# Kernel tuning notes

Measured on AMD Instinct MI355X. Metric: run time of the kernel, lower is better.

The kernel has to match this reference:

```python
import jax, jax.numpy as jnp
import numpy as np

N_NODES = 100000
N_EDGES = 3200000
D_IN = 256
D_OUT = 256


def setup_inputs() -> dict:
    key = jax.random.key(0)
    k1, k2, k3, k4, k5, k6 = jax.random.split(key, 6)
    x = jax.random.normal(k1, (N_NODES, D_IN), dtype=jnp.float32)
    edge_row = jax.random.randint(k2, (N_EDGES,), 0, N_NODES, dtype=jnp.int32)
    edge_col = jax.random.randint(k3, (N_EDGES,), 0, N_NODES, dtype=jnp.int32)
    edge_val = jax.random.uniform(k4, (N_EDGES,), dtype=jnp.float32)
    # nn.Linear params (PyTorch stores weight as [out, in]; we apply x @ W.T + b)
    bound = 1.0 / np.sqrt(D_IN)
    W = jax.random.uniform(k5, (D_OUT, D_IN), minval=-bound, maxval=bound, dtype=jnp.float32)
    b = jax.random.uniform(k6, (D_OUT,), minval=-bound, maxval=bound, dtype=jnp.float32)
    return {"x": x, "edge_row": edge_row, "edge_col": edge_col,
            "edge_val": edge_val, "W": W, "b": b}


def reference(x, edge_row, edge_col, edge_val, W, b):
    # SpMM: agg[i] = sum over edges e with row[e]==i of val[e] * x[col[e]]
    messages = edge_val[:, None] * x[edge_col]          # [E, D_in]
    agg = jax.ops.segment_sum(messages, edge_row, num_segments=N_NODES)  # [N, D_in]
    # Dense linear: agg @ W.T + b
    return jnp.einsum('nd,od->no', agg, W) + b
```

## Files before the change

kernel.cpp:

```cpp
#include <hip/hip_runtime.h>

#define THREADS 256
#define P2T 512
#define P1B 1024
#define MAXEPB 3200
#define CVTXB 1536

typedef __attribute__((ext_vector_type(8))) short short8;
typedef __attribute__((ext_vector_type(4))) float f32x4;

__device__ __forceinline__ unsigned short f2bf(float f) {
    unsigned u = __builtin_bit_cast(unsigned, f);
    return (unsigned short)((u + 0x7FFFu + ((u >> 16) & 1u)) >> 16);
}
__device__ __forceinline__ float bf2f_lo(unsigned u) { return __builtin_bit_cast(float, u << 16); }
__device__ __forceinline__ float bf2f_hi(unsigned u) { return __builtin_bit_cast(float, u & 0xFFFF0000u); }

__global__ __launch_bounds__(THREADS)
void p1_presort_kernel(const int* __restrict__ row, const int* __restrict__ col,
                       const float* __restrict__ val, int* __restrict__ gcur,
                       uint2* __restrict__ estage, int n_edges, int nbkt, int capS) {
    __shared__ int h[512];
    __shared__ int base[512];
    __shared__ int gchunk[512];
    __shared__ int curl[512];
    __shared__ int wsum[4];
    __shared__ uint2 rec[MAXEPB];
    __shared__ unsigned short rbkt[MAXEPB];

    int b = blockIdx.x, tid = threadIdx.x;
    int g = b & 7;
    int E0 = (int)((long long)b * n_edges / P1B);
    int E1 = (int)((long long)(b + 1) * n_edges / P1B);
    int cnt = E1 - E0;

    h[2 * tid] = 0; h[2 * tid + 1] = 0;
    __syncthreads();
    for (int e = E0 + tid; e < E1; e += THREADS)
        atomicAdd(&h[row[e] >> 8], 1);
    __syncthreads();
    int v0 = h[2 * tid], v1 = h[2 * tid + 1];
    int ts = v0 + v1;
    int lane = tid & 63, w = tid >> 6;
    int incl = ts;
    #pragma unroll
    for (int off = 1; off < 64; off <<= 1) {
        int t = __shfl_up(incl, off, 64);
        if (lane >= off) incl += t;
    }
    if (lane == 63) wsum[w] = incl;
    __syncthreads();
    int wo = 0;
    for (int i = 0; i < w; ++i) wo += wsum[i];
    int excl = wo + incl - ts;
    base[2 * tid] = excl;
    base[2 * tid + 1] = excl + v0;
    curl[2 * tid] = excl;
    curl[2 * tid + 1] = excl + v0;
    #pragma unroll
    for (int q = 0; q < 2; ++q) {
        int bk = 2 * tid + q;
        if (bk < nbkt) {
            int c = h[bk];
            int ro = c ? atomicAdd(&gcur[bk * 8 + g], c) : 0;
            gchunk[bk] = (bk * 8 + g) * capS + ro;
        }
    }
    __syncthreads();
    for (int e = E0 + tid; e < E1; e += THREADS) {
        int r = row[e];
        int bk = r >> 8;
        int pos = atomicAdd(&curl[bk], 1);
        rec[pos] = make_uint2(((unsigned)(r & 255) << 24) | (unsigned)col[e],
                              (unsigned)__float_as_int(val[e]));
        rbkt[pos] = (unsigned short)bk;
    }
    __syncthreads();
    for (int i = tid; i < cnt; i += THREADS) {
        int bk = rbkt[i];
        int dst = gchunk[bk] + (i - base[bk]);
        if (dst < (bk * 8 + g + 1) * capS)
            estage[dst] = rec[i];
    }
}

__global__ void cvtWX_kernel(const float* __restrict__ W, unsigned short* __restrict__ WbP,
                             const float4* __restrict__ x, uint4* __restrict__ xb, int n8) {
    int b = blockIdx.x, tid = threadIdx.x;
    if (b < 32) {
        int f = b * THREADS + tid;
        int l = f & 63, nt = (f >> 6) & 15, k0i = f >> 10;
        int r = nt * 16 + (l & 15);
        int koff = k0i * 32 + 8 * (l >> 4);
        const float4* s = reinterpret_cast<const float4*>(W + r * 256 + koff);
        float4 a = s[0], bb = s[1];
        uint4 o;
        o.x = (unsigned)f2bf(a.x) | ((unsigned)f2bf(a.y) << 16);
        o.y = (unsigned)f2bf(a.z) | ((unsigned)f2bf(a.w) << 16);
        o.z = (unsigned)f2bf(bb.x) | ((unsigned)f2bf(bb.y) << 16);
        o.w = (unsigned)f2bf(bb.z) | ((unsigned)f2bf(bb.w) << 16);
        reinterpret_cast<uint4*>(WbP)[f] = o;
    } else {
        int stride = CVTXB * THREADS;
        for (int i = (b - 32) * THREADS + tid; i < n8; i += stride) {
            float4 a = x[2 * i], bb = x[2 * i + 1];
            uint4 o;
            o.x = (unsigned)f2bf(a.x) | ((unsigned)f2bf(a.y) << 16);
            o.y = (unsigned)f2bf(a.z) | ((unsigned)f2bf(a.w) << 16);
            o.z = (unsigned)f2bf(bb.x) | ((unsigned)f2bf(bb.y) << 16);
            o.w = (unsigned)f2bf(bb.z) | ((unsigned)f2bf(bb.w) << 16);
            reinterpret_cast<uint4*>(xb)[i] = o;
        }
    }
}

__global__ void p2_sort(const uint2* __restrict__ estage, const int* __restrict__ gcur,
                        int2* __restrict__ pr, int* __restrict__ offs,
                        int capS, int n_nodes, int nbkt) {
    __shared__ int red[P2T];
    __shared__ int h[256];
    __shared__ int curh[256];
    __shared__ int wsum[4];
    __shared__ int scnt[8];
    int b = blockIdx.x, tid = threadIdx.x;

    int lim = b * 8;
    int partial = 0;
    for (int j = tid; j < lim; j += P2T) {
        int c = gcur[j];
        partial += c > capS ? capS : c;
    }
    red[tid] = partial;
    __syncthreads();
    #pragma unroll
    for (int s = P2T / 2; s > 0; s >>= 1) {
        if (tid < s) red[tid] += red[tid + s];
        __syncthreads();
    }
    int gb = red[0];
    if (tid < 8) {
        int c = gcur[b * 8 + tid];
        scnt[tid] = c > capS ? capS : c;
    }
    if (tid < 256) h[tid] = 0;
    __syncthreads();

    #pragma unroll
    for (int g = 0; g < 8; ++g) {
        int cnt = scnt[g];
        int base = (b * 8 + g) * capS;
        for (int i = tid; i < cnt; i += P2T)
            atomicAdd(&h[estage[base + i].x >> 24], 1);
    }
    __syncthreads();
    if (tid < 256) {
        int v = h[tid];
        int lane = tid & 63, w = tid >> 6;
        int incl = v;
        #pragma unroll
        for (int off = 1; off < 64; off <<= 1) {
            int t = __shfl_up(incl, off, 64);
            if (lane >= off) incl += t;
        }
        if (lane == 63) wsum[w] = incl;
        __syncthreads();
        int wo = 0;
        for (int i = 0; i < w; ++i) wo += wsum[i];
        int excl = wo + incl - v;
        int node = b * 256 + tid;
        if (node < n_nodes) offs[node] = gb + excl;
        curh[tid] = gb + excl;
    } else {
        __syncthreads();
    }
    if (b == nbkt - 1 && tid == 0) {
        int t = 0;
        #pragma unroll
        for (int g = 0; g < 8; ++g) t += scnt[g];
        offs[n_nodes] = gb + t;
    }
    __syncthreads();
    #pragma unroll
    for (int g = 0; g < 8; ++g) {
        int cnt = scnt[g];
        int base = (b * 8 + g) * capS;
        for (int i = tid; i < cnt; i += P2T) {
            uint2 p = estage[base + i];
            int q = atomicAdd(&curh[(int)(p.x >> 24)], 1);
            pr[q] = make_int2((int)(p.x & 0x00FFFFFFu), (int)p.y);
        }
    }
}

template<int OUT_BF16>
__global__ void spmm_bf16_kernel(const uint2* __restrict__ xb, const int* __restrict__ offs,
                                 const int2* __restrict__ pr, void* __restrict__ outp,
                                 int b0, int b1, int nnodes) {
    int g = blockIdx.x & 7;
    int inst = blockIdx.x >> 3;
    int bkt = b0 + g + 8 * (inst >> 6);
    if (bkt >= b1) return;
    int wid = bkt * 256 + (inst & 63) * 4 + (threadIdx.x >> 6);
    int lane = threadIdx.x & 63;
    if (wid >= nnodes) return;
    int s = offs[wid], e = offs[wid + 1];
    float a0 = 0.f, a1 = 0.f, a2 = 0.f, a3 = 0.f;
    int i = s;
    if (i < e && (i & 1)) {
        int2 p = pr[i];
        uint2 xv = xb[(size_t)p.x * 64 + lane];
        float v = __int_as_float(p.y);
        a0 = fmaf(v, bf2f_lo(xv.x), a0); a1 = fmaf(v, bf2f_hi(xv.x), a1);
        a2 = fmaf(v, bf2f_lo(xv.y), a2); a3 = fmaf(v, bf2f_hi(xv.y), a3);
        ++i;
    }
    for (; i + 8 <= e; i += 8) {
        int4 pa = *reinterpret_cast<const int4*>(pr + i);
        int4 pb = *reinterpret_cast<const int4*>(pr + i + 2);
        int4 pc = *reinterpret_cast<const int4*>(pr + i + 4);
        int4 pd = *reinterpret_cast<const int4*>(pr + i + 6);
        uint2 x0 = xb[(size_t)pa.x * 64 + lane];
        uint2 x1 = xb[(size_t)pa.z * 64 + lane];
        uint2 x2 = xb[(size_t)pb.x * 64 + lane];
        uint2 x3 = xb[(size_t)pb.z * 64 + lane];
        uint2 x4_ = xb[(size_t)pc.x * 64 + lane];
        uint2 x5 = xb[(size_t)pc.z * 64 + lane];
        uint2 x6 = xb[(size_t)pd.x * 64 + lane];
        uint2 x7 = xb[(size_t)pd.z * 64 + lane];
        float v0 = __int_as_float(pa.y), v1 = __int_as_float(pa.w);
        float v2 = __int_as_float(pb.y), v3 = __int_as_float(pb.w);
        float v4 = __int_as_float(pc.y), v5 = __int_as_float(pc.w);
        float v6 = __int_as_float(pd.y), v7 = __int_as_float(pd.w);
        a0 = fmaf(v0, bf2f_lo(x0.x), a0); a1 = fmaf(v0, bf2f_hi(x0.x), a1);
        a2 = fmaf(v0, bf2f_lo(x0.y), a2); a3 = fmaf(v0, bf2f_hi(x0.y), a3);
        a0 = fmaf(v1, bf2f_lo(x1.x), a0); a1 = fmaf(v1, bf2f_hi(x1.x), a1);
        a2 = fmaf(v1, bf2f_lo(x1.y), a2); a3 = fmaf(v1, bf2f_hi(x1.y), a3);
        a0 = fmaf(v2, bf2f_lo(x2.x), a0); a1 = fmaf(v2, bf2f_hi(x2.x), a1);
        a2 = fmaf(v2, bf2f_lo(x2.y), a2); a3 = fmaf(v2, bf2f_hi(x2.y), a3);
        a0 = fmaf(v3, bf2f_lo(x3.x), a0); a1 = fmaf(v3, bf2f_hi(x3.x), a1);
        a2 = fmaf(v3, bf2f_lo(x3.y), a2); a3 = fmaf(v3, bf2f_hi(x3.y), a3);
        a0 = fmaf(v4, bf2f_lo(x4_.x), a0); a1 = fmaf(v4, bf2f_hi(x4_.x), a1);
        a2 = fmaf(v4, bf2f_lo(x4_.y), a2); a3 = fmaf(v4, bf2f_hi(x4_.y), a3);
        a0 = fmaf(v5, bf2f_lo(x5.x), a0); a1 = fmaf(v5, bf2f_hi(x5.x), a1);
        a2 = fmaf(v5, bf2f_lo(x5.y), a2); a3 = fmaf(v5, bf2f_hi(x5.y), a3);
        a0 = fmaf(v6, bf2f_lo(x6.x), a0); a1 = fmaf(v6, bf2f_hi(x6.x), a1);
        a2 = fmaf(v6, bf2f_lo(x6.y), a2); a3 = fmaf(v6, bf2f_hi(x6.y), a3);
        a0 = fmaf(v7, bf2f_lo(x7.x), a0); a1 = fmaf(v7, bf2f_hi(x7.x), a1);
        a2 = fmaf(v7, bf2f_lo(x7.y), a2); a3 = fmaf(v7, bf2f_hi(x7.y), a3);
    }
    for (; i + 2 <= e; i += 2) {
        int4 pa = *reinterpret_cast<const int4*>(pr + i);
        uint2 x0 = xb[(size_t)pa.x * 64 + lane];
        uint2 x1 = xb[(size_t)pa.z * 64 + lane];
        float v0 = __int_as_float(pa.y), v1 = __int_as_float(pa.w);
        a0 = fmaf(v0, bf2f_lo(x0.x), a0); a1 = fmaf(v0, bf2f_hi(x0.x), a1);
        a2 = fmaf(v0, bf2f_lo(x0.y), a2); a3 = fmaf(v0, bf2f_hi(x0.y), a3);
        a0 = fmaf(v1, bf2f_lo(x1.x), a0); a1 = fmaf(v1, bf2f_hi(x1.x), a1);
        a2 = fmaf(v1, bf2f_lo(x1.y), a2); a3 = fmaf(v1, bf2f_hi(x1.y), a3);
    }
    for (; i < e; ++i) {
        int2 p = pr[i];
        uint2 xv = xb[(size_t)p.x * 64 + lane];
        float v = __int_as_float(p.y);
        a0 = fmaf(v, bf2f_lo(xv.x), a0); a1 = fmaf(v, bf2f_hi(xv.x), a1);
        a2 = fmaf(v, bf2f_lo(xv.y), a2); a3 = fmaf(v, bf2f_hi(xv.y), a3);
    }
    if (OUT_BF16) {
        ushort4 o;
        o.x = f2bf(a0); o.y = f2bf(a1); o.z = f2bf(a2); o.w = f2bf(a3);
        *reinterpret_cast<ushort4*>((unsigned short*)outp + (size_t)wid * 256 + 4 * lane) = o;
    } else {
        ((float4*)outp)[(size_t)wid * 64 + lane] = make_float4(a0, a1, a2, a3);
    }
}

__global__ void spmm_f32_kernel(const float4* __restrict__ x4, const int* __restrict__ offs,
                                const int2* __restrict__ pr, float4* __restrict__ out4,
                                int nnodes) {
    int wid = (blockIdx.x * blockDim.x + threadIdx.x) >> 6;
    int lane = threadIdx.x & 63;
    if (wid >= nnodes) return;
    int s = offs[wid], e = offs[wid + 1];
    float4 acc = make_float4(0.f, 0.f, 0.f, 0.f);
    for (int i = s; i < e; ++i) {
        int2 p = pr[i];
        float4 xv = x4[(size_t)p.x * 64 + lane];
        float v = __int_as_float(p.y);
        acc.x = fmaf(v, xv.x, acc.x); acc.y = fmaf(v, xv.y, acc.y);
        acc.z = fmaf(v, xv.z, acc.z); acc.w = fmaf(v, xv.w, acc.w);
    }
    out4[(size_t)wid * 64 + lane] = acc;
}

__launch_bounds__(256)
__global__ void gemm_direct3_kernel(const unsigned short* __restrict__ aggb,
                                    const unsigned short* __restrict__ WbP,
                                    const float* __restrict__ bias,
                                    float* __restrict__ out, int n) {
    int tid = threadIdx.x, lane = tid & 63, w = tid >> 6;
    int row0 = blockIdx.x * 128 + w * 32;
    int lr = lane & 15, lg = lane >> 4;
    const unsigned short* arow0 = aggb + (size_t)(row0 + lr) * 256 + lg * 8;
    const unsigned short* arow1 = arow0 + 16 * 256;
    short8 af0[8], af1[8];
    #pragma unroll
    for (int k = 0; k < 8; ++k) {
        af0[k] = *reinterpret_cast<const short8*>(arow0 + k * 32);
        af1[k] = *reinterpret_cast<const short8*>(arow1 + k * 32);
    }
    #pragma unroll
    for (int half = 0; half < 2; ++half) {
        f32x4 acc0[8], acc1[8];
        #pragma unroll
        for (int nt = 0; nt < 8; ++nt) {
            acc0[nt] = (f32x4){0.f, 0.f, 0.f, 0.f};
            acc1[nt] = (f32x4){0.f, 0.f, 0.f, 0.f};
        }
        #pragma unroll
        for (int k = 0; k < 8; ++k) {
            #pragma unroll
            for (int nt = 0; nt < 8; ++nt) {
                short8 bf_ = *reinterpret_cast<const short8*>(
                    &WbP[(size_t)((k * 16 + half * 8 + nt) * 64 + lane) * 8]);
                acc0[nt] = __builtin_amdgcn_mfma_f32_16x16x32_bf16(af0[k], bf_, acc0[nt], 0, 0, 0);
                acc1[nt] = __builtin_amdgcn_mfma_f32_16x16x32_bf16(af1[k], bf_, acc1[nt], 0, 0, 0);
            }
        }
        #pragma unroll
        for (int nt = 0; nt < 8; ++nt) {
            int gc = half * 128 + nt * 16 + lr;
            float bv = bias[gc];
            #pragma unroll
            for (int q = 0; q < 4; ++q) {
                int gr0 = row0 + lg * 4 + q;
                int gr1 = gr0 + 16;
                if (gr0 < n) out[(size_t)gr0 * 256 + gc] = acc0[nt][q] + bv;
                if (gr1 < n) out[(size_t)gr1 * 256 + gc] = acc1[nt][q] + bv;
            }
        }
    }
}


__global__ void zero_kernel(int* __restrict__ p, int n) {
    int i = blockIdx.x * blockDim.x + threadIdx.x;
    if (i < n) p[i] = 0;
}

__global__ void hist_part_kernel(const int* __restrict__ row, int* __restrict__ cnt,
                                 int n_edges, int n_nodes) {
    int g = blockIdx.x & 7;
    int inst = blockIdx.x >> 3;
    int ninst = gridDim.x >> 3;
    int lo = (int)(((long long)g * n_nodes) >> 3);
    int hi = (int)(((long long)(g + 1) * n_nodes) >> 3);
    int e0 = (int)(((long long)inst * n_edges) / ninst);
    int e1 = (int)(((long long)(inst + 1) * n_edges) / ninst);
    for (int e = e0 + threadIdx.x; e < e1; e += THREADS) {
        int r = row[e];
        if (r >= lo && r < hi) atomicAdd(&cnt[r], 1);
    }
}

__global__ void place_part_kernel(const int* __restrict__ row, const int* __restrict__ col,
                                  const float* __restrict__ val, int* __restrict__ cur,
                                  int2* __restrict__ pr, int n_edges, int n_nodes) {
    int g = blockIdx.x & 7;
    int inst = blockIdx.x >> 3;
    int ninst = gridDim.x >> 3;
    int lo = (int)(((long long)g * n_nodes) >> 3);
    int hi = (int)(((long long)(g + 1) * n_nodes) >> 3);
    int e0 = (int)(((long long)inst * n_edges) / ninst);
    int e1 = (int)(((long long)(inst + 1) * n_edges) / ninst);
    for (int e = e0 + threadIdx.x; e < e1; e += THREADS) {
        int r = row[e];
        if (r >= lo && r < hi) {
            int p = atomicAdd(&cur[r], 1);
            pr[p] = make_int2(col[e], __float_as_int(val[e]));
        }
    }
}

__global__ void scan1_kernel(const int* __restrict__ cnt, int* __restrict__ offs,
                             int* __restrict__ bsum, int n) {
    int tid = threadIdx.x;
    int base = blockIdx.x * 1024 + tid * 4;
    int v0 = 0, v1 = 0, v2 = 0, v3 = 0;
    if (base + 3 < n) {
        int4 v = *reinterpret_cast<const int4*>(cnt + base);
        v0 = v.x; v1 = v.y; v2 = v.z; v3 = v.w;
    } else {
        if (base + 0 < n) v0 = cnt[base + 0];
        if (base + 1 < n) v1 = cnt[base + 1];
        if (base + 2 < n) v2 = cnt[base + 2];
    }
    int ts = v0 + v1 + v2 + v3;
    int lane = tid & 63;
    int incl = ts;
    #pragma unroll
    for (int off = 1; off < 64; off <<= 1) {
        int t = __shfl_up(incl, off, 64);
        if (lane >= off) incl += t;
    }
    __shared__ int wsum[4];
    int w = tid >> 6;
    if (lane == 63) wsum[w] = incl;
    __syncthreads();
    int wo = 0;
    for (int i = 0; i < w; ++i) wo += wsum[i];
    int excl = wo + incl - ts;
    if (base + 0 < n) offs[base + 0] = excl;
    if (base + 1 < n) offs[base + 1] = excl + v0;
    if (base + 2 < n) offs[base + 2] = excl + v0 + v1;
    if (base + 3 < n) offs[base + 3] = excl + v0 + v1 + v2;
    if (tid == THREADS - 1) bsum[blockIdx.x] = wo + incl;
}

__global__ void scan2_kernel(int* __restrict__ bsum, int nb) {
    int tid = threadIdx.x;
    int base = tid * 4;
    int v0 = 0, v1 = 0, v2 = 0, v3 = 0;
    if (base + 0 < nb) v0 = bsum[base + 0];
    if (base + 1 < nb) v1 = bsum[base + 1];
    if (base + 2 < nb) v2 = bsum[base + 2];
    if (base + 3 < nb) v3 = bsum[base + 3];
    int ts = v0 + v1 + v2 + v3;
    int lane = tid & 63;
    int incl = ts;
    #pragma unroll
    for (int off = 1; off < 64; off <<= 1) {
        int t = __shfl_up(incl, off, 64);
        if (lane >= off) incl += t;
    }
    __shared__ int wsum[4];
    int w = tid >> 6;
    if (lane == 63) wsum[w] = incl;
    __syncthreads();
    int wo = 0;
    for (int i = 0; i < w; ++i) wo += wsum[i];
    int excl = wo + incl - ts;
    if (base + 0 < nb) bsum[base + 0] = excl;
    if (base + 1 < nb) bsum[base + 1] = excl + v0;
    if (base + 2 < nb) bsum[base + 2] = excl + v0 + v1;
    if (base + 3 < nb) bsum[base + 3] = excl + v0 + v1 + v2;
    if (tid == THREADS - 1) bsum[nb] = wo + incl;
}

__global__ void scan3_kernel(int* __restrict__ offs, const int* __restrict__ bsum,
                             int* __restrict__ cur, int n) {
    int i = blockIdx.x * blockDim.x + threadIdx.x;
    if (i < n) {
        int v = offs[i] + bsum[i >> 10];
        offs[i] = v;
        cur[i] = v;
    }
    if (i == 0) offs[n] = bsum[(n + 1023) >> 10];
}

__global__ void cvt_bf16_kernel(const float4* __restrict__ in, uint4* __restrict__ out, int n8) {
    int i = blockIdx.x * blockDim.x + threadIdx.x;
    if (i >= n8) return;
    float4 a = in[2 * i], b = in[2 * i + 1];
    uint4 o;
    o.x = (unsigned)f2bf(a.x) | ((unsigned)f2bf(a.y) << 16);
    o.y = (unsigned)f2bf(a.z) | ((unsigned)f2bf(a.w) << 16);
    o.z = (unsigned)f2bf(b.x) | ((unsigned)f2bf(b.y) << 16);
    o.w = (unsigned)f2bf(b.z) | ((unsigned)f2bf(b.w) << 16);
    out[i] = o;
}

__launch_bounds__(256, 2)
__global__ void gemm_mfma_kernel(float* __restrict__ out, const unsigned short* __restrict__ Wb,
                                 const float* __restrict__ bias, int nrows) {
    __shared__ unsigned short As[64][264];
    __shared__ unsigned short Ws[256][40];
    int tid = threadIdx.x;
    int rowBase = blockIdx.x * 64;

    const float4* o4 = reinterpret_cast<const float4*>(out);
    for (int it = tid; it < 64 * 64; it += 256) {
        int r = it >> 6, c = it & 63;
        float4 v = make_float4(0.f, 0.f, 0.f, 0.f);
        int gr = rowBase + r;
        if (gr < nrows) v = o4[(size_t)gr * 64 + c];
        ushort4 w;
        w.x = f2bf(v.x); w.y = f2bf(v.y); w.z = f2bf(v.z); w.w = f2bf(v.w);
        *reinterpret_cast<ushort4*>(&As[r][c * 4]) = w;
    }

    int w = tid >> 6, lane = tid & 63;
    int lr = lane & 15, lg = lane >> 4;
    f32x4 acc[16];
    #pragma unroll
    for (int nt = 0; nt < 16; ++nt) acc[nt] = (f32x4){0.f, 0.f, 0.f, 0.f};

    for (int k0 = 0; k0 < 256; k0 += 32) {
        __syncthreads();
        for (int it = tid; it < 1024; it += 256) {
            int r = it >> 2, c = it & 3;
            uint4 v = *reinterpret_cast<const uint4*>(Wb + (size_t)r * 256 + k0 + c * 8);
            *reinterpret_cast<uint4*>(&Ws[r][c * 8]) = v;
        }
        __syncthreads();
        short8 af = *reinterpret_cast<const short8*>(&As[w * 16 + lr][k0 + 8 * lg]);
        #pragma unroll
        for (int nt = 0; nt < 16; ++nt) {
            short8 bf_ = *reinterpret_cast<const short8*>(&Ws[nt * 16 + lr][8 * lg]);
            acc[nt] = __builtin_amdgcn_mfma_f32_16x16x32_bf16(af, bf_, acc[nt], 0, 0, 0);
        }
    }

    #pragma unroll
    for (int nt = 0; nt < 16; ++nt) {
        int gc = nt * 16 + lr;
        float bv = bias[gc];
        #pragma unroll
        for (int q = 0; q < 4; ++q) {
            int gr = rowBase + w * 16 + lg * 4 + q;
            if (gr < nrows) out[(size_t)gr * 256 + gc] = acc[nt][q] + bv;
        }
    }
}


extern "C" void kernel_launch(void* const* d_in, const int* in_sizes, int n_in,
                              void* d_out, int out_size, void* d_ws, size_t ws_size,
                              hipStream_t stream) {
    const float* x     = (const float*)d_in[0];
    const int*   erow  = (const int*)d_in[1];
    const int*   ecol  = (const int*)d_in[2];
    const float* evalv = (const float*)d_in[3];
    const float* W     = (const float*)d_in[4];
    const float* bias  = (const float*)d_in[5];
    float* out = (float*)d_out;

    int n_nodes = in_sizes[0] / 256;
    int n_edges = in_sizes[1];

    int nbkt = (n_nodes + 255) >> 8;
    int avg8 = n_edges / (8 * (nbkt > 0 ? nbkt : 1)) + 1;
    int capS = avg8 + avg8 / 8 + 512;

    size_t A = (size_t)((n_nodes + 63) & ~63) + 64;
    int* offs  = (int*)d_ws;
    int* gcur  = offs + A;
    unsigned short* WbP = (unsigned short*)(gcur + 4096);
    int2* pr = (int2*)(WbP + 65536);
    int* after_pr = (int*)(pr + n_edges);

    size_t est_ints  = (size_t)nbkt * 8 * capS * 2;
    size_t aggb_ints = (size_t)n_nodes * 128 + 32768;
    size_t xb_ints   = (size_t)n_nodes * 128;
    size_t alias_ints = est_ints > aggb_ints ? est_ints : aggb_ints;
    size_t head_ints = (size_t)(after_pr - (int*)d_ws);
    size_t need_new = (head_ints + alias_ints + xb_ints) * 4;
    bool new_ok = (nbkt <= 512) && (nbkt >= 1) && (n_nodes <= (1 << 24)) &&
                  (n_edges <= P1B * (MAXEPB - 64)) && ws_size >= need_new;

    if (new_ok) {
        uint2* estage = (uint2*)after_pr;
        unsigned short* aggb = (unsigned short*)after_pr;
        unsigned short* xb = (unsigned short*)(after_pr + alias_ints);

        hipMemsetAsync(gcur, 0, 4096 * sizeof(int), stream);
        int n8 = n_nodes * 32;
        cvtWX_kernel<<<32 + CVTXB, THREADS, 0, stream>>>(
            W, WbP, (const float4*)x, (uint4*)xb, n8);
        p1_presort_kernel<<<P1B, THREADS, 0, stream>>>(
            erow, ecol, evalv, gcur, estage, n_edges, nbkt, capS);
        p2_sort<<<nbkt, P2T, 0, stream>>>(estage, gcur, pr, offs, capS, n_nodes, nbkt);

        int grid = 8 * ((nbkt + 7) / 8) * 64;
        spmm_bf16_kernel<1><<<grid, THREADS, 0, stream>>>(
            (const uint2*)xb, offs, pr, aggb, 0, nbkt, n_nodes);
        int gb = (n_nodes + 127) / 128;
        gemm_direct3_kernel<<<gb, THREADS, 0, stream>>>(aggb, WbP, bias, out, n_nodes);
    } else {
        int nb = (n_nodes + 1023) >> 10;
        size_t Af = (size_t)((n_nodes + 63) & ~63);
        int* cnt   = (int*)d_ws;
        int* offsf = cnt + Af;
        int* cur   = offsf + Af;
        int* bsum  = cur + Af;
        int* wbase = bsum + (((size_t)nb + 64) & ~63ull);
        unsigned short* Wbf = (unsigned short*)wbase;
        int2* prf  = (int2*)(Wbf + 65536);
        int* aft   = (int*)(prf + n_edges);
        unsigned short* xbf = (unsigned short*)aft;
        size_t need_old = (size_t)((char*)(xbf + (size_t)n_nodes * 256) - (char*)d_ws);
        bool told = ws_size >= need_old;

        zero_kernel<<<(n_nodes + THREADS - 1) / THREADS, THREADS, 0, stream>>>(cnt, n_nodes);
        hist_part_kernel<<<2048, THREADS, 0, stream>>>(erow, cnt, n_edges, n_nodes);
        scan1_kernel<<<nb, THREADS, 0, stream>>>(cnt, offsf, bsum, n_nodes);
        scan2_kernel<<<1, THREADS, 0, stream>>>(bsum, nb);
        scan3_kernel<<<(n_nodes + THREADS - 1) / THREADS, THREADS, 0, stream>>>(offsf, bsum, cur, n_nodes);
        place_part_kernel<<<2048, THREADS, 0, stream>>>(erow, ecol, evalv, cur, prf, n_edges, n_nodes);
        cvt_bf16_kernel<<<32, THREADS, 0, stream>>>((const float4*)W, (uint4*)Wbf, 65536 / 8);

        int gb = (n_nodes + 63) / 64;
        if (told) {
            int n8 = n_nodes * 32;
            cvt_bf16_kernel<<<(n8 + THREADS - 1) / THREADS, THREADS, 0, stream>>>(
                (const float4*)x, (uint4*)xbf, n8);
            int nbf = (n_nodes + 255) / 256;
            int gridf = 8 * ((nbf + 7) / 8) * 64;
            spmm_bf16_kernel<0><<<gridf, THREADS, 0, stream>>>(
                (const uint2*)xbf, offsf, prf, out, 0, nbf, n_nodes);
        } else {
            int spmm_blocks_f = (n_nodes + 3) / 4;
            spmm_f32_kernel<<<spmm_blocks_f, THREADS, 0, stream>>>(
                (const float4*)x, offsf, prf, (float4*)out, n_nodes);
        }
        gemm_mfma_kernel<<<gb, THREADS, 0, stream>>>(out, Wbf, bias, n_nodes);
    }
}
```

Baseline: 422.9 us.

## Slice bf16 features into 16 column slabs for cache-resident sliced SpMM

Converts x to bf16 in a feature-sliced layout of 16 slabs, each holding 16 columns (32 bytes per node), so every slab is about 3.2 MB and can stay in L2/LLC. The SpMM runs per slice, with 8 edges handled in parallel per wave and a shuffle reduction at the end. Its output uses the same sliced layout, and the GEMM's A-fragment loads are changed to read it. The aim is to turn random 512-byte row gathers from a 51 MB table into cache-friendly 32-byte gathers. In exchange, the edge list is re-read 16 times and the reduction adds shuffle overhead.

```diff
diff --git a/kernel.cpp b/kernel.cpp
--- a/kernel.cpp
+++ b/kernel.cpp
@@ -85,7 +85,8 @@
 }
 
 __global__ void cvtWX_kernel(const float* __restrict__ W, unsigned short* __restrict__ WbP,
-                             const float4* __restrict__ x, uint4* __restrict__ xb, int n8) {
+                             const float* __restrict__ x, unsigned short* __restrict__ xs,
+                             int n_nodes) {
     int b = blockIdx.x, tid = threadIdx.x;
     if (b < 32) {
         int f = b * THREADS + tid;
@@ -102,14 +103,23 @@
         reinterpret_cast<uint4*>(WbP)[f] = o;
     } else {
         int stride = CVTXB * THREADS;
-        for (int i = (b - 32) * THREADS + tid; i < n8; i += stride) {
-            float4 a = x[2 * i], bb = x[2 * i + 1];
-            uint4 o;
-            o.x = (unsigned)f2bf(a.x) | ((unsigned)f2bf(a.y) << 16);
-            o.y = (unsigned)f2bf(a.z) | ((unsigned)f2bf(a.w) << 16);
-            o.z = (unsigned)f2bf(bb.x) | ((unsigned)f2bf(bb.y) << 16);
-            o.w = (unsigned)f2bf(bb.z) | ((unsigned)f2bf(bb.w) << 16);
-            reinterpret_cast<uint4*>(xb)[i] = o;
+        int total = n_nodes * 16;
+        for (int idx = (b - 32) * THREADS + tid; idx < total; idx += stride) {
+            int s = idx / n_nodes;
+            int n = idx - s * n_nodes;
+            const float4* xr = reinterpret_cast<const float4*>(x) + (size_t)n * 64 + s * 4;
+            float4 a = xr[0], bb = xr[1], c = xr[2], d = xr[3];
+            uint4 o0, o1;
+            o0.x = (unsigned)f2bf(a.x) | ((unsigned)f2bf(a.y) << 16);
+            o0.y = (unsigned)f2bf(a.z) | ((unsigned)f2bf(a.w) << 16);
+            o0.z = (unsigned)f2bf(bb.x) | ((unsigned)f2bf(bb.y) << 16);
+            o0.w = (unsigned)f2bf(bb.z) | ((unsigned)f2bf(bb.w) << 16);
+            o1.x = (unsigned)f2bf(c.x) | ((unsigned)f2bf(c.y) << 16);
+            o1.y = (unsigned)f2bf(c.z) | ((unsigned)f2bf(c.w) << 16);
+            o1.z = (unsigned)f2bf(d.x) | ((unsigned)f2bf(d.y) << 16);
+            o1.w = (unsigned)f2bf(d.z) | ((unsigned)f2bf(d.w) << 16);
+            uint4* dst = reinterpret_cast<uint4*>(xs) + (size_t)idx * 2;
+            dst[0] = o0; dst[1] = o1;
         }
     }
 }
@@ -192,121 +202,75 @@
     }
 }
 
-template<int OUT_BF16>
-__global__ void spmm_bf16_kernel(const uint2* __restrict__ xb, const int* __restrict__ offs,
-                                 const int2* __restrict__ pr, void* __restrict__ outp,
-                                 int b0, int b1, int nnodes) {
+__global__ __launch_bounds__(THREADS)
+void spmm_sliced_kernel(const unsigned* __restrict__ xs, const int* __restrict__ offs,
+                        const int2* __restrict__ pr, unsigned short* __restrict__ aggs,
+                        int n_nodes, int bps) {
     int g = blockIdx.x & 7;
     int inst = blockIdx.x >> 3;
-    int bkt = b0 + g + 8 * (inst >> 6);
-    if (bkt >= b1) return;
-    int wid = bkt * 256 + (inst & 63) * 4 + (threadIdx.x >> 6);
-    int lane = threadIdx.x & 63;
-    if (wid >= nnodes) return;
-    int s = offs[wid], e = offs[wid + 1];
-    float a0 = 0.f, a1 = 0.f, a2 = 0.f, a3 = 0.f;
-    int i = s;
-    if (i < e && (i & 1)) {
-        int2 p = pr[i];
-        uint2 xv = xb[(size_t)p.x * 64 + lane];
-        float v = __int_as_float(p.y);
-        a0 = fmaf(v, bf2f_lo(xv.x), a0); a1 = fmaf(v, bf2f_hi(xv.x), a1);
-        a2 = fmaf(v, bf2f_lo(xv.y), a2); a3 = fmaf(v, bf2f_hi(xv.y), a3);
-        ++i;
-    }
-    for (; i + 8 <= e; i += 8) {
-        int4 pa = *reinterpret_cast<const int4*>(pr + i);
-        int4 pb = *reinterpret_cast<const int4*>(pr + i + 2);
-        int4 pc = *reinterpret_cast<const int4*>(pr + i + 4);
-        int4 pd = *reinterpret_cast<const int4*>(pr + i + 6);
-        uint2 x0 = xb[(size_t)pa.x * 64 + lane];
-        uint2 x1 = xb[(size_t)pa.z * 64 + lane];
-        uint2 x2 = xb[(size_t)pb.x * 64 + lane];
-        uint2 x3 = xb[(size_t)pb.z * 64 + lane];
-        uint2 x4_ = xb[(size_t)pc.x * 64 + lane];
-        uint2 x5 = xb[(size_t)pc.z * 64 + lane];
-        uint2 x6 = xb[(size_t)pd.x * 64 + lane];
-        uint2 x7 = xb[(size_t)pd.z * 64 + lane];
-        float v0 = __int_as_float(pa.y), v1 = __int_as_float(pa.w);
-        float v2 = __int_as_float(pb.y), v3 = __int_as_float(pb.w);
-        float v4 = __int_as_float(pc.y), v5 = __int_as_float(pc.w);
-        float v6 = __int_as_float(pd.y), v7 = __int_as_float(pd.w);
-        a0 = fmaf(v0, bf2f_lo(x0.x), a0); a1 = fmaf(v0, bf2f_hi(x0.x), a1);
-        a2 = fmaf(v0, bf2f_lo(x0.y), a2); a3 = fmaf(v0, bf2f_hi(x0.y), a3);
-        a0 = fmaf(v1, bf2f_lo(x1.x), a0); a1 = fmaf(v1, bf2f_hi(x1.x), a1);
-        a2 = fmaf(v1, bf2f_lo(x1.y), a2); a3 = fmaf(v1, bf2f_hi(x1.y), a3);
-        a0 = fmaf(v2, bf2f_lo(x2.x), a0); a1 = fmaf(v2, bf2f_hi(x2.x), a1);
-        a2 = fmaf(v2, bf2f_lo(x2.y), a2); a3 = fmaf(v2, bf2f_hi(x2.y), a3);
-        a0 = fmaf(v3, bf2f_lo(x3.x), a0); a1 = fmaf(v3, bf2f_hi(x3.x), a1);
-        a2 = fmaf(v3, bf2f_lo(x3.y), a2); a3 = fmaf(v3, bf2f_hi(x3.y), a3);
-        a0 = fmaf(v4, bf2f_lo(x4_.x), a0); a1 = fmaf(v4, bf2f_hi(x4_.x), a1);
-        a2 = fmaf(v4, bf2f_lo(x4_.y), a2); a3 = fmaf(v4, bf2f_hi(x4_.y), a3);
-        a0 = fmaf(v5, bf2f_lo(x5.x), a0); a1 = fmaf(v5, bf2f_hi(x5.x), a1);
-        a2 = fmaf(v5, bf2f_lo(x5.y), a2); a3 = fmaf(v5, bf2f_hi(x5.y), a3);
-        a0 = fmaf(v6, bf2f_lo(x6.x), a0); a1 = fmaf(v6, bf2f_hi(x6.x), a1);
-        a2 = fmaf(v6, bf2f_lo(x6.y), a2); a3 = fmaf(v6, bf2f_hi(x6.y), a3);
-        a0 = fmaf(v7, bf2f_lo(x7.x), a0); a1 = fmaf(v7, bf2f_hi(x7.x), a1);
-        a2 = fmaf(v7, bf2f_lo(x7.y), a2); a3 = fmaf(v7, bf2f_hi(x7.y), a3);
-    }
-    for (; i + 2 <= e; i += 2) {
-        int4 pa = *reinterpret_cast<const int4*>(pr + i);
-        uint2 x0 = xb[(size_t)pa.x * 64 + lane];
-        uint2 x1 = xb[(size_t)pa.z * 64 + lane];
-        float v0 = __int_as_float(pa.y), v1 = __int_as_float(pa.w);
-        a0 = fmaf(v0, bf2f_lo(x0.x), a0); a1 = fmaf(v0, bf2f_hi(x0.x), a1);
-        a2 = fmaf(v0, bf2f_lo(x0.y), a2); a3 = fmaf(v0, bf2f_hi(x0.y), a3);
-        a0 = fmaf(v1, bf2f_lo(x1.x), a0); a1 = fmaf(v1, bf2f_hi(x1.x), a1);
-        a2 = fmaf(v1, bf2f_lo(x1.y), a2); a3 = fmaf(v1, bf2f_hi(x1.y), a3);
-    }
-    for (; i < e; ++i) {
-        int2 p = pr[i];
-        uint2 xv = xb[(size_t)p.x * 64 + lane];
-        float v = __int_as_float(p.y);
-        a0 = fmaf(v, bf2f_lo(xv.x), a0); a1 = fmaf(v, bf2f_hi(xv.x), a1);
-        a2 = fmaf(v, bf2f_lo(xv.y), a2); a3 = fmaf(v, bf2f_hi(xv.y), a3);
-    }
-    if (OUT_BF16) {
-        ushort4 o;
-        o.x = f2bf(a0); o.y = f2bf(a1); o.z = f2bf(a2); o.w = f2bf(a3);
-        *reinterpret_cast<ushort4*>((unsigned short*)outp + (size_t)wid * 256 + 4 * lane) = o;
-    } else {
-        ((float4*)outp)[(size_t)wid * 64 + lane] = make_float4(a0, a1, a2, a3);
-    }
-}
-
-__global__ void spmm_f32_kernel(const float4* __restrict__ x4, const int* __restrict__ offs,
-                                const int2* __restrict__ pr, float4* __restrict__ out4,
-                                int nnodes) {
-    int wid = (blockIdx.x * blockDim.x + threadIdx.x) >> 6;
-    int lane = threadIdx.x & 63;
-    if (wid >= nnodes) return;
-    int s = offs[wid], e = offs[wid + 1];
-    float4 acc = make_float4(0.f, 0.f, 0.f, 0.f);
-    for (int i = s; i < e; ++i) {
-        int2 p = pr[i];
-        float4 xv = x4[(size_t)p.x * 64 + lane];
-        float v = __int_as_float(p.y);
-        acc.x = fmaf(v, xv.x, acc.x); acc.y = fmaf(v, xv.y, acc.y);
-        acc.z = fmaf(v, xv.z, acc.z); acc.w = fmaf(v, xv.w, acc.w);
-    }
-    out4[(size_t)wid * 64 + lane] = acc;
+    int ph = inst >= bps;
+    int sl = 2 * g + ph;
+    int nblk = inst - (ph ? bps : 0);
+    int wid = threadIdx.x >> 6, lane = threadIdx.x & 63;
+    int grp = lane >> 3, fl = lane & 7;
+    const unsigned* xsl = xs + (size_t)sl * n_nodes * 8;
+    unsigned* asl = reinterpret_cast<unsigned*>(aggs) + (size_t)sl * n_nodes * 8;
+    int n0 = nblk * 32 + wid * 8;
+    for (int ni = 0; ni < 8; ++ni) {
+        int n = n0 + ni;
+        if (n >= n_nodes) return;
+        int s = offs[n], e = offs[n + 1];
+        float a0 = 0.f, a1 = 0.f;
+        int i = s;
+        for (; i + 16 <= e; i += 16) {
+            long long q0 = __builtin_nontemporal_load(
+                reinterpret_cast<const long long*>(pr + i + grp));
+            long long q1 = __builtin_nontemporal_load(
+                reinterpret_cast<const long long*>(pr + i + 8 + grp));
+            int c0 = (int)(unsigned)q0, c1 = (int)(unsigned)q1;
+            float v0 = __int_as_float((int)(q0 >> 32));
+            float v1 = __int_as_float((int)(q1 >> 32));
+            unsigned x0 = xsl[(size_t)c0 * 8 + fl];
+            unsigned x1 = xsl[(size_t)c1 * 8 + fl];
+            a0 = fmaf(v0, bf2f_lo(x0), a0); a1 = fmaf(v0, bf2f_hi(x0), a1);
+            a0 = fmaf(v1, bf2f_lo(x1), a0); a1 = fmaf(v1, bf2f_hi(x1), a1);
+        }
+        for (; i < e; i += 8) {
+            int ei = i + grp;
+            long long q = 0;
+            if (ei < e)
+                q = __builtin_nontemporal_load(
+                    reinterpret_cast<const long long*>(pr + ei));
+            int c = (int)(unsigned)q;
+            float v = __int_as_float((int)(q >> 32));
+            unsigned xv = xsl[(size_t)c * 8 + fl];
+            a0 = fmaf(v, bf2f_lo(xv), a0); a1 = fmaf(v, bf2f_hi(xv), a1);
+        }
+        a0 += __shfl_xor(a0, 8);  a1 += __shfl_xor(a1, 8);
+        a0 += __shfl_xor(a0, 16); a1 += __shfl_xor(a1, 16);
+        a0 += __shfl_xor(a0, 32); a1 += __shfl_xor(a1, 32);
+        if (lane < 8) {
+            unsigned ov = (unsigned)f2bf(a0) | ((unsigned)f2bf(a1) << 16);
+            __builtin_nontemporal_store(ov, asl + (size_t)n * 8 + fl);
+        }
+    }
 }
 
 __launch_bounds__(256)
-__global__ void gemm_direct3_kernel(const unsigned short* __restrict__ aggb,
+__global__ void gemm_direct3_kernel(const unsigned short* __restrict__ aggs,
                                     const unsigned short* __restrict__ WbP,
                                     const float* __restrict__ bias,
                                     float* __restrict__ out, int n) {
     int tid = threadIdx.x, lane = tid & 63, w = tid >> 6;
     int row0 = blockIdx.x * 128 + w * 32;
     int lr = lane & 15, lg = lane >> 4;
-    const unsigned short* arow0 = aggb + (size_t)(row0 + lr) * 256 + lg * 8;
-    const unsigned short* arow1 = arow0 + 16 * 256;
     short8 af0[8], af1[8];
     #pragma unroll
     for (int k = 0; k < 8; ++k) {
-        af0[k] = *reinterpret_cast<const short8*>(arow0 + k * 32);
-        af1[k] = *reinterpret_cast<const short8*>(arow1 + k * 32);
+        size_t sidx = (size_t)(2 * k + (lg >> 1)) * n + (row0 + lr);
+        int off = 8 * (lg & 1);
+        af0[k] = *reinterpret_cast<const short8*>(aggs + sidx * 16 + off);
+        af1[k] = *reinterpret_cast<const short8*>(aggs + (sidx + 16) * 16 + off);
     }
     #pragma unroll
     for (int half = 0; half < 2; ++half) {
@@ -469,6 +433,49 @@
     out[i] = o;
 }
 
+template<int OUT_BF16>
+__global__ void spmm_bf16_kernel(const uint2* __restrict__ xb, const int* __restrict__ offs,
+                                 const int2* __restrict__ pr, void* __restrict__ outp,
+                                 int nnodes) {
+    int wid = (blockIdx.x * blockDim.x + threadIdx.x) >> 6;
+    int lane = threadIdx.x & 63;
+    if (wid >= nnodes) return;
+    int s = offs[wid], e = offs[wid + 1];
+    float a0 = 0.f, a1 = 0.f, a2 = 0.f, a3 = 0.f;
+    for (int i = s; i < e; ++i) {
+        int2 p = pr[i];
+        uint2 xv = xb[(size_t)p.x * 64 + lane];
+        float v = __int_as_float(p.y);
+        a0 = fmaf(v, bf2f_lo(xv.x), a0); a1 = fmaf(v, bf2f_hi(xv.x), a1);
+        a2 = fmaf(v, bf2f_lo(xv.y), a2); a3 = fmaf(v, bf2f_hi(xv.y), a3);
+    }
+    if (OUT_BF16) {
+        ushort4 o;
+        o.x = f2bf(a0); o.y = f2bf(a1); o.z = f2bf(a2); o.w = f2bf(a3);
+        *reinterpret_cast<ushort4*>((unsigned short*)outp + (size_t)wid * 256 + 4 * lane) = o;
+    } else {
+        ((float4*)outp)[(size_t)wid * 64 + lane] = make_float4(a0, a1, a2, a3);
+    }
+}
+
+__global__ void spmm_f32_kernel(const float4* __restrict__ x4, const int* __restrict__ offs,
+                                const int2* __restrict__ pr, float4* __restrict__ out4,
+                                int nnodes) {
+    int wid = (blockIdx.x * blockDim.x + threadIdx.x) >> 6;
+    int lane = threadIdx.x & 63;
+    if (wid >= nnodes) return;
+    int s = offs[wid], e = offs[wid + 1];
+    float4 acc = make_float4(0.f, 0.f, 0.f, 0.f);
+    for (int i = s; i < e; ++i) {
+        int2 p = pr[i];
+        float4 xv = x4[(size_t)p.x * 64 + lane];
+        float v = __int_as_float(p.y);
+        acc.x = fmaf(v, xv.x, acc.x); acc.y = fmaf(v, xv.y, acc.y);
+        acc.z = fmaf(v, xv.z, acc.z); acc.w = fmaf(v, xv.w, acc.w);
+    }
+    out4[(size_t)wid * 64 + lane] = acc;
+}
+
 __launch_bounds__(256, 2)
 __global__ void gemm_mfma_kernel(float* __restrict__ out, const unsigned short* __restrict__ Wb,
                                  const float* __restrict__ bias, int nrows) {
@@ -559,22 +566,21 @@
 
     if (new_ok) {
         uint2* estage = (uint2*)after_pr;
-        unsigned short* aggb = (unsigned short*)after_pr;
-        unsigned short* xb = (unsigned short*)(after_pr + alias_ints);
+        unsigned short* aggs = (unsigned short*)after_pr;
+        unsigned short* xs = (unsigned short*)(after_pr + alias_ints);
 
         hipMemsetAsync(gcur, 0, 4096 * sizeof(int), stream);
-        int n8 = n_nodes * 32;
-        cvtWX_kernel<<<32 + CVTXB, THREADS, 0, stream>>>(
-            W, WbP, (const float4*)x, (uint4*)xb, n8);
+        cvtWX_kernel<<<32 + CVTXB, THREADS, 0, stream>>>(W, WbP, x, xs, n_nodes);
         p1_presort_kernel<<<P1B, THREADS, 0, stream>>>(
             erow, ecol, evalv, gcur, estage, n_edges, nbkt, capS);
         p2_sort<<<nbkt, P2T, 0, stream>>>(estage, gcur, pr, offs, capS, n_nodes, nbkt);
 
-        int grid = 8 * ((nbkt + 7) / 8) * 64;
-        spmm_bf16_kernel<1><<<grid, THREADS, 0, stream>>>(
-            (const uint2*)xb, offs, pr, aggb, 0, nbkt, n_nodes);
+        int bps = (n_nodes + 31) / 32;
+        spmm_sliced_kernel<<<16 * bps, THREADS, 0, stream>>>(
+            (const unsigned*)xs, offs, pr, aggs, n_nodes, bps);
+
         int gb = (n_nodes + 127) / 128;
-        gemm_direct3_kernel<<<gb, THREADS, 0, stream>>>(aggb, WbP, bias, out, n_nodes);
+        gemm_direct3_kernel<<<gb, THREADS, 0, stream>>>(aggs, WbP, bias, out, n_nodes);
     } else {
         int nb = (n_nodes + 1023) >> 10;
         size_t Af = (size_t)((n_nodes + 63) & ~63);
@@ -603,13 +609,12 @@
             int n8 = n_nodes * 32;
             cvt_bf16_kernel<<<(n8 + THREADS - 1) / THREADS, THREADS, 0, stream>>>(
                 (const float4*)x, (uint4*)xbf, n8);
-            int nbf = (n_nodes + 255) / 256;
-            int gridf = 8 * ((nbf + 7) / 8) * 64;
-            spmm_bf16_kernel<0><<<gridf, THREADS, 0, stream>>>(
-                (const uint2*)xbf, offsf, prf, out, 0, nbf, n_nodes);
+            int spmm_blocks = (n_nodes + 3) / 4;
+            spmm_bf16_kernel<0><<<spmm_blocks, THREADS, 0, stream>>>(
+                (const uint2*)xbf, offsf, prf, out, n_nodes);
         } else {
-            int spmm_blocks_f = (n_nodes + 3) / 4;
-            spmm_f32_kernel<<<spmm_blocks_f, THREADS, 0, stream>>>(
+            int spmm_blocks = (n_nodes + 3) / 4;
+            spmm_f32_kernel<<<spmm_blocks, THREADS, 0, stream>>>(
                 (const float4*)x, offsf, prf, (float4*)out, n_nodes);
         }
         gemm_mfma_kernel<<<gb, THREADS, 0, stream>>>(out, Wbf, bias, n_nodes);
```

Result: slower. 932.6 us (+120.5%).
